# Kernel tuning notes

Measured on AMD Instinct MI355X. Metric: run time of the kernel, lower is better.

The kernel has to match this reference:

```python
import jax, jax.numpy as jnp
import numpy as np

N_NODES = 100000
N_EDGES = 1600000
N_GRAPHS = 256
IN_C = 64
HID = 128
OUT = 128
BN_EPS = 1e-5


def setup_inputs() -> dict:
    key = jax.random.key(0)
    ks = jax.random.split(key, 24)
    x = jax.random.normal(ks[0], (N_NODES, IN_C), jnp.float32)
    edge_index = jax.random.randint(ks[1], (2, N_EDGES), 0, N_NODES, dtype=jnp.int64 if jax.config.jax_enable_x64 else jnp.int32)
    batch = jnp.sort(jax.random.randint(ks[2], (N_NODES,), 0, N_GRAPHS))

    def lin(k, i, o):
        return (jax.random.normal(k, (i, o), jnp.float32) / np.float32(np.sqrt(i)))

    d = {"x": x, "edge_index": edge_index, "batch": batch}
    in_dims = [IN_C, HID, HID]
    for l in range(3):
        d[f"w1_{l}"] = lin(ks[3 + 6 * l], in_dims[l], HID)
        d[f"b1_{l}"] = jnp.zeros((HID,), jnp.float32)
        d[f"w2_{l}"] = lin(ks[4 + 6 * l], HID, HID)
        d[f"b2_{l}"] = jnp.zeros((HID,), jnp.float32)
        d[f"gamma_{l}"] = jnp.ones((HID,), jnp.float32)
        d[f"beta_{l}"] = jnp.zeros((HID,), jnp.float32)
    d["proj_w"] = lin(ks[22], HID, OUT)
    d["proj_b"] = jnp.zeros((OUT,), jnp.float32)
    return d


def _gin_forward(x, edge_index, batch, layers, proj_w, proj_b):
    src, dst = edge_index[0], edge_index[1]
    h = x
    for (w1, b1, w2, b2, g, b) in layers:
        # GINConv (eps=0, aggr='add'): MLP(h_i + sum_{j->i} h_j)
        agg = jax.ops.segment_sum(h[src], dst, num_segments=h.shape[0])
        z = h + agg
        z = jax.nn.relu(z @ w1 + b1) @ w2 + b2
        # BatchNorm1d, training mode (biased batch stats)
        mean = z.mean(axis=0)
        var = z.var(axis=0)
        z = (z - mean) * jax.lax.rsqrt(var + BN_EPS) * g + b
        h = jax.nn.relu(z)
    # global_mean_pool over graph ids
    s = jax.ops.segment_sum(h, batch, num_segments=N_GRAPHS)
    cnt = jax.ops.segment_sum(jnp.ones((h.shape[0], 1), h.dtype), batch, num_segments=N_GRAPHS)
    hg = s / jnp.maximum(cnt, 1.0)
    return hg @ proj_w + proj_b


def reference(x, edge_index, batch,
              w1_0, b1_0, w2_0, b2_0, gamma_0, beta_0,
              w1_1, b1_1, w2_1, b2_1, gamma_1, beta_1,
              w1_2, b1_2, w2_2, b2_2, gamma_2, beta_2,
              proj_w, proj_b):
    layers = [
        (w1_0, b1_0, w2_0, b2_0, gamma_0, beta_0),
        (w1_1, b1_1, w2_1, b2_1, gamma_1, beta_1),
        (w1_2, b1_2, w2_2, b2_2, gamma_2, beta_2),
    ]
    return _gin_forward(x, edge_index, batch, layers, proj_w, proj_b)
```

## Files before the change

### kernel.cpp

```cpp
#include <hip/hip_runtime.h>

#define N_NODES 100000
#define N_EDGES 1600000
#define N_GRAPHS 256
#define HID 128
#define BN_EPS 1e-5f

#define NT 1563
#define EB 4096
#define RB 391
#define PB 6250

typedef __bf16 bf16x8 __attribute__((ext_vector_type(8)));
typedef __bf16 bf16x4 __attribute__((ext_vector_type(4)));
typedef __bf16 bf16x2 __attribute__((ext_vector_type(2)));
typedef float f32x4 __attribute__((ext_vector_type(4)));

__global__ __launch_bounds__(256) void setup_kernel(
    const float* __restrict__ x, __bf16* __restrict__ xb,
    const float* __restrict__ wa, const float* __restrict__ wb,
    const float* __restrict__ wc, const float* __restrict__ wd,
    const float* __restrict__ we, const float* __restrict__ wf,
    __bf16* __restrict__ wt,
    const int* __restrict__ batch, int* __restrict__ counts) {
  int b = blockIdx.x;
  if (b < 6250) {
    int idx = b * 256 + threadIdx.x;
    if (idx >= N_NODES * 16) return;
    f32x4 v = ((const f32x4*)x)[idx];
    bf16x4 o = {(__bf16)v[0], (__bf16)v[1], (__bf16)v[2], (__bf16)v[3]};
    ((bf16x4*)xb)[idx] = o;
  } else if (b < 6250 + 352) {
    int idx = (b - 6250) * 256 + threadIdx.x;
    if (idx >= 90112) return;
    const float* w;
    int K, local;
    if (idx < 8192) { w = wa; K = 64; local = idx; }
    else {
      int s = (idx - 8192) / 16384;
      local = (idx - 8192) - s * 16384;
      K = 128;
      w = (s == 0) ? wb : (s == 1) ? wc : (s == 2) ? wd : (s == 3) ? we : wf;
    }
    int n = local / K, k = local - n * K;
    wt[idx] = (__bf16)w[k * 128 + n];
  } else {
    int t = (b - 6602) * 256 + threadIdx.x;
    int r0 = t * 64;
    if (r0 >= N_NODES) return;
    int rend = min(r0 + 64, N_NODES);
    int curg = batch[r0], cnt = 0;
    for (int r = r0; r < rend; r++) {
      int g = batch[r];
      if (g != curg) {
        atomicAdd(&counts[curg], cnt);
        curg = g;
        cnt = 1;
      } else {
        cnt++;
      }
    }
    atomicAdd(&counts[curg], cnt);
  }
}

__global__ __launch_bounds__(256) void tile_hist_kernel(const int* __restrict__ ei,
                                                        int* __restrict__ tcnt) {
  __shared__ int hist[NT];
  int t = threadIdx.x;
  for (int i = t; i < NT; i += 256) hist[i] = 0;
  __syncthreads();
  int base = blockIdx.x * EB;
#pragma unroll 4
  for (int i = 0; i < EB / 256; i++) {
    int e = base + i * 256 + t;
    if (e < N_EDGES) atomicAdd(&hist[ei[N_EDGES + e] >> 6], 1);
  }
  __syncthreads();
  for (int i = t; i < NT; i += 256) {
    int h = hist[i];
    if (h) atomicAdd(&tcnt[i], h);
  }
}

__global__ __launch_bounds__(256) void tile_scan_kernel(const int* __restrict__ tcnt,
                                                        int* __restrict__ tstart,
                                                        int* __restrict__ gcursor) {
  __shared__ int ps[256];
  int t = threadIdx.x;
  const int CH = (NT + 255) / 256;
  int lo = t * CH, hi = min(lo + CH, NT);
  int s = 0;
  for (int i = lo; i < hi; i++) s += tcnt[i];
  ps[t] = s;
  __syncthreads();
  for (int off = 1; off < 256; off <<= 1) {
    int v = ps[t];
    int u = (t >= off) ? ps[t - off] : 0;
    __syncthreads();
    ps[t] = v + u;
    __syncthreads();
  }
  int base = (t == 0) ? 0 : ps[t - 1];
  for (int i = lo; i < hi; i++) {
    tstart[i] = base;
    gcursor[i] = base;
    base += tcnt[i];
  }
  if (t == 0) tstart[NT] = N_EDGES;
}

__global__ __launch_bounds__(256) void reorder2_kernel(const int* __restrict__ ei,
                                                       int* __restrict__ gcursor,
                                                       int* __restrict__ epack) {
  __shared__ int hist[NT];
  int t = threadIdx.x;
  for (int i = t; i < NT; i += 256) hist[i] = 0;
  __syncthreads();
  int base = blockIdx.x * EB;
#pragma unroll 4
  for (int i = 0; i < EB / 256; i++) {
    int e = base + i * 256 + t;
    if (e < N_EDGES) atomicAdd(&hist[ei[N_EDGES + e] >> 6], 1);
  }
  __syncthreads();
  for (int i = t; i < NT; i += 256) {
    int h = hist[i];
    if (h) hist[i] = atomicAdd(&gcursor[i], h);
  }
  __syncthreads();
#pragma unroll 4
  for (int i = 0; i < EB / 256; i++) {
    int e = base + i * 256 + t;
    if (e < N_EDGES) {
      int d = ei[N_EDGES + e];
      int s = ei[e];
      int pos = atomicAdd(&hist[d >> 6], 1);
      epack[pos] = (s << 6) | (d & 63);
    }
  }
}

__global__ __launch_bounds__(256) void row_sort_kernel(const int* __restrict__ tstart,
                                                       const int* __restrict__ epack,
                                                       int* __restrict__ starts,
                                                       int* __restrict__ srcs) {
  __shared__ int cnt[64];
  __shared__ int rbase[65];
  __shared__ int rofs[64];
  int t = threadIdx.x, b = blockIdx.x;
  int ts = tstart[b], te = tstart[b + 1];
  if (t < 64) cnt[t] = 0;
  __syncthreads();
  for (int i = ts + t; i < te; i += 256) atomicAdd(&cnt[epack[i] & 63], 1);
  __syncthreads();
  if (t == 0) {
    int a = 0;
    for (int r = 0; r < 64; r++) { rbase[r] = a; a += cnt[r]; }
    rbase[64] = a;
  }
  __syncthreads();
  if (t < 64) rofs[t] = ts + rbase[t];
  if (t <= 64) {
    int gr = b * 64 + t;
    if (gr <= N_NODES) starts[gr] = ts + rbase[t];
  }
  __syncthreads();
  for (int i = ts + t; i < te; i += 256) {
    int p = epack[i];
    int pos = atomicAdd(&rofs[p & 63], 1);
    srcs[pos] = p >> 6;
  }
}

template <int C, bool BN>
__global__ __launch_bounds__(256) void gather_kernel(const __bf16* __restrict__ h,
                                                     const float* __restrict__ accum,
                                                     const float* __restrict__ gamma,
                                                     const float* __restrict__ beta,
                                                     const int* __restrict__ starts,
                                                     const int* __restrict__ srcs,
                                                     __bf16* __restrict__ z) {
  const int lane = threadIdx.x & 63;
  const int row = __builtin_amdgcn_readfirstlane(blockIdx.x * 4 + (threadIdx.x >> 6));
  const int e0 = starts[row], e1 = starts[row + 1];

  if constexpr (C == 128) {
    float a0 = 0.f, a1 = 0.f, b0 = 0.f, b1 = 0.f;
    if constexpr (BN) {
      const int c0 = lane * 2, c1 = c0 + 1;
      const float invN = 1.f / (float)N_NODES;
      float m0 = accum[c0] * invN, m1 = accum[c1] * invN;
      float v0 = accum[HID + c0] * invN - m0 * m0;
      float v1 = accum[HID + c1] * invN - m1 * m1;
      a0 = gamma[c0] * rsqrtf(v0 + BN_EPS);
      a1 = gamma[c1] * rsqrtf(v1 + BN_EPS);
      b0 = beta[c0] - m0 * a0;
      b1 = beta[c1] - m1 * a1;
    }
#define ACCBN(vv, ss)                                                  \
    do {                                                               \
      if constexpr (BN) {                                              \
        ss.x += fmaxf(fmaf(a0, (float)(vv)[0], b0), 0.f);              \
        ss.y += fmaxf(fmaf(a1, (float)(vv)[1], b1), 0.f);              \
      } else {                                                         \
        ss.x += (float)(vv)[0];                                        \
        ss.y += (float)(vv)[1];                                        \
      }                                                                \
    } while (0)
    float2 s0 = {0.f, 0.f}, s1 = {0.f, 0.f}, s2 = {0.f, 0.f}, s3 = {0.f, 0.f};
    int e = e0;
    for (; e + 3 < e1; e += 4) {
      int i0 = srcs[e];
      int i1 = srcs[e + 1];
      int i2 = srcs[e + 2];
      int i3 = srcs[e + 3];
      bf16x2 v0 = *(const bf16x2*)(h + (size_t)i0 * 128 + lane * 2);
      bf16x2 v1 = *(const bf16x2*)(h + (size_t)i1 * 128 + lane * 2);
      bf16x2 v2 = *(const bf16x2*)(h + (size_t)i2 * 128 + lane * 2);
      bf16x2 v3 = *(const bf16x2*)(h + (size_t)i3 * 128 + lane * 2);
      ACCBN(v0, s0);
      ACCBN(v1, s1);
      ACCBN(v2, s2);
      ACCBN(v3, s3);
    }
    for (; e < e1; e++) {
      int i0 = srcs[e];
      bf16x2 vv = *(const bf16x2*)(h + (size_t)i0 * 128 + lane * 2);
      ACCBN(vv, s0);
    }
    bf16x2 sv = *(const bf16x2*)(h + (size_t)row * 128 + lane * 2);
    ACCBN(sv, s0);
    float tx = (s0.x + s1.x) + (s2.x + s3.x);
    float ty = (s0.y + s1.y) + (s2.y + s3.y);
    bf16x2 o = {(__bf16)tx, (__bf16)ty};
    *(bf16x2*)(z + (size_t)row * 128 + lane * 2) = o;
#undef ACCBN
  } else {
    float s0 = 0.f, s1 = 0.f, s2 = 0.f, s3 = 0.f;
    int e = e0;
    for (; e + 3 < e1; e += 4) {
      int i0 = srcs[e];
      int i1 = srcs[e + 1];
      int i2 = srcs[e + 2];
      int i3 = srcs[e + 3];
      float v0 = (float)h[(size_t)i0 * 64 + lane];
      float v1 = (float)h[(size_t)i1 * 64 + lane];
      float v2 = (float)h[(size_t)i2 * 64 + lane];
      float v3 = (float)h[(size_t)i3 * 64 + lane];
      s0 += v0; s1 += v1; s2 += v2; s3 += v3;
    }
    for (; e < e1; e++) {
      int i0 = srcs[e];
      s0 += (float)h[(size_t)i0 * 64 + lane];
    }
    s0 += (float)h[(size_t)row * 64 + lane];
    float tot = (s0 + s1) + (s2 + s3);
    z[(size_t)row * 64 + lane] = (__bf16)tot;
  }
}

template <int CIN>
__global__ __launch_bounds__(64) void mlp_kernel(
    const __bf16* __restrict__ z, const __bf16* __restrict__ w1t,
    const float* __restrict__ b1, const __bf16* __restrict__ w2t,
    const float* __restrict__ b2, __bf16* __restrict__ u,
    float* __restrict__ part) {
  constexpr int TS = HID + 8;
  __shared__ __align__(16) __bf16 sm[16 * TS];

  const int lane = threadIdx.x;
  const int l16 = lane & 15;
  const int quad = lane >> 4;
  const int rowbase = blockIdx.x * 16;

  const f32x4 zero4 = {0.f, 0.f, 0.f, 0.f};
  f32x4 acc[8];

  {
    bf16x8 af[CIN / 32];
    const __bf16* ap = z + (size_t)(rowbase + l16) * CIN + quad * 8;
#pragma unroll
    for (int ks = 0; ks < CIN / 32; ks++) af[ks] = *(const bf16x8*)(ap + ks * 32);
#pragma unroll
    for (int ct = 0; ct < 8; ct++) acc[ct] = zero4;
#pragma unroll
    for (int ks = 0; ks < CIN / 32; ks++) {
#pragma unroll
      for (int ct = 0; ct < 8; ct++) {
        bf16x8 bfr = *(const bf16x8*)(w1t + (ct * 16 + l16) * CIN + ks * 32 + quad * 8);
        acc[ct] = __builtin_amdgcn_mfma_f32_16x16x32_bf16(af[ks], bfr, acc[ct], 0, 0, 0);
      }
    }
#pragma unroll
    for (int ct = 0; ct < 8; ct++) {
      int col = ct * 16 + l16;
      float bias = b1[col];
#pragma unroll
      for (int r = 0; r < 4; r++) {
        float v = acc[ct][r] + bias;
        sm[(quad * 4 + r) * TS + col] = (__bf16)(v > 0.f ? v : 0.f);
      }
    }
  }

  {
#pragma unroll
    for (int ct = 0; ct < 8; ct++) acc[ct] = zero4;
    const __bf16* arowp = sm + l16 * TS + quad * 8;
#pragma unroll
    for (int ks = 0; ks < HID / 32; ks++) {
      bf16x8 af = *(const bf16x8*)(arowp + ks * 32);
#pragma unroll
      for (int ct = 0; ct < 8; ct++) {
        bf16x8 bfr = *(const bf16x8*)(w2t + (ct * 16 + l16) * HID + ks * 32 + quad * 8);
        acc[ct] = __builtin_amdgcn_mfma_f32_16x16x32_bf16(af, bfr, acc[ct], 0, 0, 0);
      }
    }
  }

#pragma unroll
  for (int ct = 0; ct < 8; ct++) {
    int col = ct * 16 + l16;
    float bias = b2[col];
    float s = 0.f, q = 0.f;
#pragma unroll
    for (int r = 0; r < 4; r++) {
      float v = acc[ct][r] + bias;
      __bf16 bv = (__bf16)v;
      u[(size_t)(rowbase + quad * 4 + r) * HID + col] = bv;
      float fv = (float)bv;
      s += fv;
      q += fv * fv;
    }
    s += __shfl_xor(s, 16);
    s += __shfl_xor(s, 32);
    q += __shfl_xor(q, 16);
    q += __shfl_xor(q, 32);
    if (quad == 0) {
      part[(size_t)blockIdx.x * 256 + col] = s;
      part[(size_t)blockIdx.x * 256 + HID + col] = q;
    }
  }
}

__global__ __launch_bounds__(256) void reduce_part_kernel(const float* __restrict__ part,
                                                          float* __restrict__ accum) {
  int t = threadIdx.x;
  float s = 0.f;
  for (int r = blockIdx.x; r < PB; r += gridDim.x)
    s += part[(size_t)r * 256 + t];
  atomicAdd(&accum[t], s);
}

__global__ __launch_bounds__(128) void bn_apply_pool_kernel(const __bf16* __restrict__ u,
                                                            const float* __restrict__ accum,
                                                            const float* __restrict__ gamma,
                                                            const float* __restrict__ beta,
                                                            const int* __restrict__ batch,
                                                            float* __restrict__ pool) {
  int c = threadIdx.x;
  int r0 = blockIdx.x * 64;
  if (r0 >= N_NODES) return;
  int rend = min(r0 + 64, N_NODES);
  const float invN = 1.f / (float)N_NODES;
  float mean = accum[c] * invN;
  float var = accum[HID + c] * invN - mean * mean;
  float a = gamma[c] * rsqrtf(var + BN_EPS);
  float b = beta[c] - mean * a;
  float accv = 0.f;
  int curg = -1;
  for (int r = r0; r < rend; r++) {
    int g = batch[r];
    if (g != curg) {
      if (curg >= 0) atomicAdd(&pool[curg * HID + c], accv);
      curg = g;
      accv = 0.f;
    }
    float v = (float)u[(size_t)r * HID + c];
    v = v * a + b;
    accv += (v > 0.f ? v : 0.f);
  }
  if (curg >= 0) atomicAdd(&pool[curg * HID + c], accv);
}

__global__ __launch_bounds__(128) void pool_proj_kernel(const float* __restrict__ pool,
                                                        const int* __restrict__ counts,
                                                        const float* __restrict__ pw,
                                                        const float* __restrict__ pb,
                                                        float* __restrict__ out) {
  int g = blockIdx.x;
  int c = threadIdx.x;
  __shared__ float hg[HID];
  float cnt = (float)max(counts[g], 1);
  hg[c] = pool[g * HID + c] / cnt;
  __syncthreads();
  float acc = pb[c];
#pragma unroll 8
  for (int k = 0; k < HID; k++) acc += hg[k] * pw[k * HID + c];
  out[g * HID + c] = acc;
}

extern "C" void kernel_launch(void* const* d_in, const int* in_sizes, int n_in,
                              void* d_out, int out_size, void* d_ws, size_t ws_size,
                              hipStream_t stream) {
  (void)in_sizes; (void)n_in; (void)out_size; (void)ws_size;
  const float* x = (const float*)d_in[0];
  const int* ei = (const int*)d_in[1];
  const int* batch = (const int*)d_in[2];
  const float* w1[3] = {(const float*)d_in[3], (const float*)d_in[9], (const float*)d_in[15]};
  const float* b1[3] = {(const float*)d_in[4], (const float*)d_in[10], (const float*)d_in[16]};
  const float* w2[3] = {(const float*)d_in[5], (const float*)d_in[11], (const float*)d_in[17]};
  const float* b2[3] = {(const float*)d_in[6], (const float*)d_in[12], (const float*)d_in[18]};
  const float* gm[3] = {(const float*)d_in[7], (const float*)d_in[13], (const float*)d_in[19]};
  const float* bt[3] = {(const float*)d_in[8], (const float*)d_in[14], (const float*)d_in[20]};
  const float* pw = (const float*)d_in[21];
  const float* pb = (const float*)d_in[22];
  float* out = (float*)d_out;

  char* ws = (char*)d_ws;
  __bf16* bufA = (__bf16*)ws;        ws += (size_t)N_NODES * HID * 2;
  __bf16* bufB = (__bf16*)ws;        ws += (size_t)N_NODES * HID * 2;
  __bf16* bufC = (__bf16*)ws;        ws += (size_t)N_NODES * HID * 2;
  __bf16* z0 = (__bf16*)ws;          ws += (size_t)N_NODES * 64 * 2;
  __bf16* xb = (__bf16*)ws;          ws += (size_t)N_NODES * 64 * 2;
  int* srcs = (int*)ws;              ws += (size_t)N_EDGES * 4;
  int* epack = (int*)ws;             ws += (size_t)N_EDGES * 4;
  int* starts = (int*)ws;            ws += (size_t)(N_NODES + 1) * 4;
  int* tcnt = (int*)ws;              ws += NT * 4;
  int* tstart = (int*)ws;            ws += (NT + 1) * 4;
  int* gcursor = (int*)ws;           ws += NT * 4;
  ws = (char*)(((uintptr_t)ws + 63) & ~(uintptr_t)63);
  float* part = (float*)ws;          ws += (size_t)PB * 256 * 4;
  __bf16* wt_all = (__bf16*)ws;      ws += 90112 * 2;
  ws = (char*)(((uintptr_t)ws + 63) & ~(uintptr_t)63);
  float* accum = (float*)ws;         ws += 3 * 256 * 4;
  float* pool = (float*)ws;          ws += N_GRAPHS * HID * 4;
  int* counts = (int*)ws;            ws += N_GRAPHS * 4;

  __bf16* w1t0 = wt_all;
  __bf16* w2t0 = wt_all + 8192;
  __bf16* w1t1 = wt_all + 24576;
  __bf16* w2t1 = wt_all + 40960;
  __bf16* w1t2 = wt_all + 57344;
  __bf16* w2t2 = wt_all + 73728;

  float* acc0 = accum;
  float* acc1 = accum + 256;
  float* acc2 = accum + 512;

  const int gat_blocks = (N_NODES + 3) / 4;

  hipMemsetAsync(accum, 0, 3 * 256 * 4 + (size_t)N_GRAPHS * HID * 4 + N_GRAPHS * 4, stream);
  hipMemsetAsync(tcnt, 0, NT * 4, stream);

  setup_kernel<<<6609, 256, 0, stream>>>(x, xb, w1[0], w2[0], w1[1], w2[1],
                                         w1[2], w2[2], wt_all, batch, counts);

  tile_hist_kernel<<<RB, 256, 0, stream>>>(ei, tcnt);
  tile_scan_kernel<<<1, 256, 0, stream>>>(tcnt, tstart, gcursor);
  reorder2_kernel<<<RB, 256, 0, stream>>>(ei, gcursor, epack);
  row_sort_kernel<<<NT, 256, 0, stream>>>(tstart, epack, starts, srcs);

  gather_kernel<64, false><<<gat_blocks, 256, 0, stream>>>(xb, nullptr, nullptr, nullptr,
                                                           starts, srcs, z0);
  mlp_kernel<64><<<PB, 64, 0, stream>>>(z0, w1t0, b1[0], w2t0, b2[0], bufA, part);
  reduce_part_kernel<<<128, 256, 0, stream>>>(part, acc0);

  gather_kernel<128, true><<<gat_blocks, 256, 0, stream>>>(bufA, acc0, gm[0], bt[0],
                                                           starts, srcs, bufC);
  mlp_kernel<128><<<PB, 64, 0, stream>>>(bufC, w1t1, b1[1], w2t1, b2[1], bufB, part);
  reduce_part_kernel<<<128, 256, 0, stream>>>(part, acc1);

  gather_kernel<128, true><<<gat_blocks, 256, 0, stream>>>(bufB, acc1, gm[1], bt[1],
                                                           starts, srcs, bufC);
  mlp_kernel<128><<<PB, 64, 0, stream>>>(bufC, w1t2, b1[2], w2t2, b2[2], bufA, part);
  reduce_part_kernel<<<128, 256, 0, stream>>>(part, acc2);

  bn_apply_pool_kernel<<<NT, 128, 0, stream>>>(bufA, acc2, gm[2], bt[2], batch, pool);

  pool_proj_kernel<<<N_GRAPHS, 128, 0, stream>>>(pool, counts, pw, pb, out);
}
```

Baseline: 612.8 us.

## Process 64 rows per MLP block to reuse weight fragments across four M-tiles

Each mlp_kernel wavefront now handles 64 rows instead of 16, loading each weight fragment once and applying it to four MFMA row tiles. This cuts weight reloads per row by a factor of four and reduces the number of partial-stat blocks. The output is staged through shared memory so stores are coalesced 16-byte writes, and BN sums are computed column-wise from that buffer. The cost is much higher register pressure (32 accumulator vectors) and a serial 64-row stats loop. The grid launch and PB must match 1563 blocks, and the last block is partial.

After: 507.9 us. -17.1%, faster.

```diff
diff --git a/kernel.cpp b/kernel.cpp
--- a/kernel.cpp
+++ b/kernel.cpp
@@ -9,7 +9,7 @@
 #define NT 1563
 #define EB 4096
 #define RB 391
-#define PB 6250
+#define PB 1563
 
 typedef __bf16 bf16x8 __attribute__((ext_vector_type(8)));
 typedef __bf16 bf16x4 __attribute__((ext_vector_type(4)));
@@ -261,35 +261,42 @@
 }
 
 template <int CIN>
-__global__ __launch_bounds__(64) void mlp_kernel(
+__global__ __launch_bounds__(64, 2) void mlp_kernel(
     const __bf16* __restrict__ z, const __bf16* __restrict__ w1t,
     const float* __restrict__ b1, const __bf16* __restrict__ w2t,
     const float* __restrict__ b2, __bf16* __restrict__ u,
     float* __restrict__ part) {
   constexpr int TS = HID + 8;
-  __shared__ __align__(16) __bf16 sm[16 * TS];
+  __shared__ __align__(16) __bf16 sm[64 * TS];
 
   const int lane = threadIdx.x;
   const int l16 = lane & 15;
   const int quad = lane >> 4;
-  const int rowbase = blockIdx.x * 16;
+  const int rowbase = blockIdx.x * 64;
+  const int nvalid = min(64, N_NODES - rowbase);
 
   const f32x4 zero4 = {0.f, 0.f, 0.f, 0.f};
-  f32x4 acc[8];
+  f32x4 acc[8][4];
 
   {
-    bf16x8 af[CIN / 32];
-    const __bf16* ap = z + (size_t)(rowbase + l16) * CIN + quad * 8;
-#pragma unroll
-    for (int ks = 0; ks < CIN / 32; ks++) af[ks] = *(const bf16x8*)(ap + ks * 32);
-#pragma unroll
-    for (int ct = 0; ct < 8; ct++) acc[ct] = zero4;
+#pragma unroll
+    for (int ct = 0; ct < 8; ct++)
+#pragma unroll
+      for (int m = 0; m < 4; m++) acc[ct][m] = zero4;
 #pragma unroll
     for (int ks = 0; ks < CIN / 32; ks++) {
+      bf16x8 af[4];
+#pragma unroll
+      for (int m = 0; m < 4; m++) {
+        int row = min(rowbase + m * 16 + l16, N_NODES - 1);
+        af[m] = *(const bf16x8*)(z + (size_t)row * CIN + ks * 32 + quad * 8);
+      }
 #pragma unroll
       for (int ct = 0; ct < 8; ct++) {
         bf16x8 bfr = *(const bf16x8*)(w1t + (ct * 16 + l16) * CIN + ks * 32 + quad * 8);
-        acc[ct] = __builtin_amdgcn_mfma_f32_16x16x32_bf16(af[ks], bfr, acc[ct], 0, 0, 0);
+#pragma unroll
+        for (int m = 0; m < 4; m++)
+          acc[ct][m] = __builtin_amdgcn_mfma_f32_16x16x32_bf16(af[m], bfr, acc[ct][m], 0, 0, 0);
       }
     }
 #pragma unroll
@@ -297,24 +304,32 @@
       int col = ct * 16 + l16;
       float bias = b1[col];
 #pragma unroll
-      for (int r = 0; r < 4; r++) {
-        float v = acc[ct][r] + bias;
-        sm[(quad * 4 + r) * TS + col] = (__bf16)(v > 0.f ? v : 0.f);
-      }
+      for (int m = 0; m < 4; m++)
+#pragma unroll
+        for (int r = 0; r < 4; r++) {
+          float v = acc[ct][m][r] + bias;
+          sm[(m * 16 + quad * 4 + r) * TS + col] = (__bf16)(v > 0.f ? v : 0.f);
+        }
     }
   }
 
   {
 #pragma unroll
-    for (int ct = 0; ct < 8; ct++) acc[ct] = zero4;
-    const __bf16* arowp = sm + l16 * TS + quad * 8;
+    for (int ct = 0; ct < 8; ct++)
+#pragma unroll
+      for (int m = 0; m < 4; m++) acc[ct][m] = zero4;
 #pragma unroll
     for (int ks = 0; ks < HID / 32; ks++) {
-      bf16x8 af = *(const bf16x8*)(arowp + ks * 32);
+      bf16x8 af[4];
+#pragma unroll
+      for (int m = 0; m < 4; m++)
+        af[m] = *(const bf16x8*)(sm + (m * 16 + l16) * TS + ks * 32 + quad * 8);
 #pragma unroll
       for (int ct = 0; ct < 8; ct++) {
         bf16x8 bfr = *(const bf16x8*)(w2t + (ct * 16 + l16) * HID + ks * 32 + quad * 8);
-        acc[ct] = __builtin_amdgcn_mfma_f32_16x16x32_bf16(af, bfr, acc[ct], 0, 0, 0);
+#pragma unroll
+        for (int m = 0; m < 4; m++)
+          acc[ct][m] = __builtin_amdgcn_mfma_f32_16x16x32_bf16(af[m], bfr, acc[ct][m], 0, 0, 0);
       }
     }
   }
@@ -323,24 +338,30 @@
   for (int ct = 0; ct < 8; ct++) {
     int col = ct * 16 + l16;
     float bias = b2[col];
-    float s = 0.f, q = 0.f;
-#pragma unroll
-    for (int r = 0; r < 4; r++) {
-      float v = acc[ct][r] + bias;
-      __bf16 bv = (__bf16)v;
-      u[(size_t)(rowbase + quad * 4 + r) * HID + col] = bv;
-      float fv = (float)bv;
-      s += fv;
-      q += fv * fv;
-    }
-    s += __shfl_xor(s, 16);
-    s += __shfl_xor(s, 32);
-    q += __shfl_xor(q, 16);
-    q += __shfl_xor(q, 32);
-    if (quad == 0) {
-      part[(size_t)blockIdx.x * 256 + col] = s;
-      part[(size_t)blockIdx.x * 256 + HID + col] = q;
-    }
+#pragma unroll
+    for (int m = 0; m < 4; m++)
+#pragma unroll
+      for (int r = 0; r < 4; r++)
+        sm[(m * 16 + quad * 4 + r) * TS + col] = (__bf16)(acc[ct][m][r] + bias);
+  }
+
+  for (int f = lane; f < nvalid * 16; f += 64) {
+    int r = f >> 4, c8 = f & 15;
+    bf16x8 v = *(const bf16x8*)(sm + r * TS + c8 * 8);
+    *(bf16x8*)(u + (size_t)(rowbase + r) * HID + c8 * 8) = v;
+  }
+
+  {
+    float s0 = 0.f, q0 = 0.f, s1 = 0.f, q1 = 0.f;
+    for (int r = 0; r < nvalid; r++) {
+      bf16x2 v = *(const bf16x2*)(sm + r * TS + lane * 2);
+      float f0 = (float)v[0], f1 = (float)v[1];
+      s0 += f0; q0 += f0 * f0;
+      s1 += f1; q1 += f1 * f1;
+    }
+    float2 sp = {s0, s1}, qp = {q0, q1};
+    *(float2*)(part + (size_t)blockIdx.x * 256 + lane * 2) = sp;
+    *(float2*)(part + (size_t)blockIdx.x * 256 + HID + lane * 2) = qp;
   }
 }
 
```
